# Performance work log

Measured on AMD Instinct MI355X. Metric: run time of the kernel, lower is better.

## Reference

```python
import jax, jax.numpy as jnp
import numpy as np

N = 8192  # num_nodes
E = 8192  # num_edges (== N so self-loops sit on the diagonal)
C = 256   # in_channels
ALPHA = 0.1
BETA = 0.5


def setup_inputs() -> dict:
    key = jax.random.key(0)
    k1, k2, k3 = jax.random.split(key, 3)
    x_0 = jax.random.normal(k1, (N, C), dtype=jnp.float32)
    # binary hypergraph incidence with self-loops on the diagonal
    mask = (jax.random.uniform(k2, (N, E)) < 0.004).astype(jnp.float32)
    idx = jnp.arange(N)
    incidence_1 = mask.at[idx, idx].set(1.0)
    # torch Linear(C, C, bias=False) weight, Kaiming-uniform-ish scale
    W = jax.random.normal(k3, (C, C), dtype=jnp.float32) / jnp.sqrt(C)
    return {"x_0": x_0, "incidence_1": incidence_1, "W": W}


def reference(x_0, incidence_1, W):
    # 1) edge aggregation: m_{0->1} = B^T x  -> [E, C]
    m_0_1 = incidence_1.T @ x_0
    # degree normalization (matches diag/to_dense math without materializing diag)
    node_degree = jnp.sum(incidence_1, axis=1)                      # [N]
    edge_degree = (node_degree @ incidence_1) / jnp.sum(incidence_1, axis=0)  # [E]
    # 2) node aggregation with 1/sqrt(d_z), 1/sqrt(d_x) scaling
    m_1_0 = (incidence_1 @ (m_0_1 / jnp.sqrt(edge_degree)[:, None])) \
            / jnp.sqrt(node_degree)[:, None]                        # [N, C]
    # 3) skip + learned update (x_skip defaults to x_0)
    x_combined = (1.0 - ALPHA) * m_1_0 + ALPHA * x_0
    return (1.0 - BETA) * x_combined + BETA * (x_combined @ W.T)
```

## Files before the change

### kernel.cpp

```cpp
#include <hip/hip_runtime.h>
#include <hip/hip_bf16.h>

#define NN 8192
#define NE 8192
#define CC 256
#define CAP 128

typedef __attribute__((ext_vector_type(8))) short bf16x8;
typedef __attribute__((ext_vector_type(4))) float f32x4;

static __device__ __forceinline__ ushort f2b(float f) {
    unsigned u = __float_as_uint(f);
    return (ushort)((u + 0x7fffu + ((u >> 16) & 1u)) >> 16);
}
static __device__ __forceinline__ float b2f(ushort u) {
    return __uint_as_float((unsigned)u << 16);
}

__global__ __launch_bounds__(256) void k1_scan(const float* __restrict__ B,
                                               const float* __restrict__ x0,
                                               const float* __restrict__ W,
                                               ushort* __restrict__ x0b,
                                               ushort* __restrict__ Wb,
                                               int* __restrict__ csr,
                                               int* __restrict__ row_cnt,
                                               int* __restrict__ col_cnt,
                                               int* __restrict__ csc,
                                               float* __restrict__ edge_wsum) {
    {
        int i = blockIdx.x * 1024 + threadIdx.x * 4;
        float4 v = *(const float4*)(x0 + i);
        ushort4 u; u.x = f2b(v.x); u.y = f2b(v.y); u.z = f2b(v.z); u.w = f2b(v.w);
        *(ushort4*)(x0b + i) = u;
        if (blockIdx.x < 64) {
            float4 w = *(const float4*)(W + i);
            ushort4 uw; uw.x = f2b(w.x); uw.y = f2b(w.y); uw.z = f2b(w.z); uw.w = f2b(w.w);
            *(ushort4*)(Wb + i) = uw;
        }
    }
    const int wave = threadIdx.x >> 6;
    const int lane = threadIdx.x & 63;
    const int row  = blockIdx.x * 4 + wave;
    const float4* rp = (const float4*)(B + (size_t)row * NE);
    int* outp = csr + (size_t)row * CAP;
    const unsigned long long mlt = (1ull << lane) - 1ull;
    int base = 0;
    for (int it = 0; it < NE / 256; ++it) {
        float4 v = rp[it * 64 + lane];
        unsigned long long bx = __ballot(v.x != 0.f);
        unsigned long long by = __ballot(v.y != 0.f);
        unsigned long long bz = __ballot(v.z != 0.f);
        unsigned long long bw = __ballot(v.w != 0.f);
        if (!(bx | by | bz | bw)) continue;
        int tx = __popcll(bx), ty = __popcll(by), tz = __popcll(bz), tw = __popcll(bw);
        int e0 = (it * 64 + lane) * 4;
        int p;
        if (v.x != 0.f) { p = base + __popcll(bx & mlt);                if (p < CAP) outp[p] = e0;     }
        if (v.y != 0.f) { p = base + tx + __popcll(by & mlt);           if (p < CAP) outp[p] = e0 + 1; }
        if (v.z != 0.f) { p = base + tx + ty + __popcll(bz & mlt);      if (p < CAP) outp[p] = e0 + 2; }
        if (v.w != 0.f) { p = base + tx + ty + tz + __popcll(bw & mlt); if (p < CAP) outp[p] = e0 + 3; }
        base += tx + ty + tz + tw;
    }
    const int cnt = base < CAP ? base : CAP;
    if (lane == 0) row_cnt[row] = cnt;
    const float deg = (float)cnt;
    for (int i = lane; i < cnt; i += 64) {
        int e = outp[i];
        int pos = atomicAdd(&col_cnt[e], 1);
        if (pos < CAP) csc[(size_t)e * CAP + pos] = row;
        atomicAdd(&edge_wsum[e], deg);
    }
}

__global__ __launch_bounds__(256) void k4_edge_agg(const ushort* __restrict__ x0b,
                                                   const int* __restrict__ csc,
                                                   const int* __restrict__ col_cnt,
                                                   const float* __restrict__ edge_wsum,
                                                   ushort* __restrict__ m01s) {
    const int wave = threadIdx.x >> 6;
    const int lane = threadIdx.x & 63;
    const int e = blockIdx.x * 4 + wave;
    int cnt = col_cnt[e]; if (cnt > CAP) cnt = CAP;
    const float er = rsqrtf(edge_wsum[e] / (float)cnt);
    const int* cp = csc + (size_t)e * CAP;
    const int idx = cp[lane];
    const ushort* xb = x0b + lane * 4;
    float ax = 0.f, ay = 0.f, az = 0.f, aw = 0.f;
    float bx = 0.f, by = 0.f, bz = 0.f, bw = 0.f;
    const int lim = cnt < 64 ? cnt : 64;
    int i = 0;
    for (; i + 2 <= lim; i += 2) {
        int n0 = __shfl(idx, i), n1 = __shfl(idx, i + 1);
        ushort4 a = *(const ushort4*)(xb + (size_t)n0 * CC);
        ushort4 b = *(const ushort4*)(xb + (size_t)n1 * CC);
        ax += b2f(a.x); ay += b2f(a.y); az += b2f(a.z); aw += b2f(a.w);
        bx += b2f(b.x); by += b2f(b.y); bz += b2f(b.z); bw += b2f(b.w);
    }
    if (i < lim) {
        int n = __shfl(idx, i);
        ushort4 a = *(const ushort4*)(xb + (size_t)n * CC);
        ax += b2f(a.x); ay += b2f(a.y); az += b2f(a.z); aw += b2f(a.w);
    }
    for (int j = 64; j < cnt; ++j) {
        int n = cp[j];
        ushort4 a = *(const ushort4*)(xb + (size_t)n * CC);
        ax += b2f(a.x); ay += b2f(a.y); az += b2f(a.z); aw += b2f(a.w);
    }
    ushort4 r;
    r.x = f2b((ax + bx) * er); r.y = f2b((ay + by) * er);
    r.z = f2b((az + bz) * er); r.w = f2b((aw + bw) * er);
    *(ushort4*)(m01s + (size_t)e * CC + lane * 4) = r;
}

__global__ __launch_bounds__(256) void k5_node_agg(const ushort* __restrict__ x0b,
                                                   const ushort* __restrict__ m01s,
                                                   const int* __restrict__ csr,
                                                   const int* __restrict__ row_cnt,
                                                   ushort* __restrict__ xcb) {
    const int wave = threadIdx.x >> 6;
    const int lane = threadIdx.x & 63;
    const int n = blockIdx.x * 4 + wave;
    const int cnt = row_cnt[n];
    const float nr = rsqrtf((float)cnt);
    const int* ep = csr + (size_t)n * CAP;
    const int idx = ep[lane];
    const ushort* mb = m01s + lane * 4;
    float ax = 0.f, ay = 0.f, az = 0.f, aw = 0.f;
    float bx = 0.f, by = 0.f, bz = 0.f, bw = 0.f;
    const int lim = cnt < 64 ? cnt : 64;
    int i = 0;
    for (; i + 2 <= lim; i += 2) {
        int e0 = __shfl(idx, i), e1 = __shfl(idx, i + 1);
        ushort4 a = *(const ushort4*)(mb + (size_t)e0 * CC);
        ushort4 b = *(const ushort4*)(mb + (size_t)e1 * CC);
        ax += b2f(a.x); ay += b2f(a.y); az += b2f(a.z); aw += b2f(a.w);
        bx += b2f(b.x); by += b2f(b.y); bz += b2f(b.z); bw += b2f(b.w);
    }
    if (i < lim) {
        int e0 = __shfl(idx, i);
        ushort4 a = *(const ushort4*)(mb + (size_t)e0 * CC);
        ax += b2f(a.x); ay += b2f(a.y); az += b2f(a.z); aw += b2f(a.w);
    }
    for (int j = 64; j < cnt; ++j) {
        int e0 = ep[j];
        ushort4 a = *(const ushort4*)(mb + (size_t)e0 * CC);
        ax += b2f(a.x); ay += b2f(a.y); az += b2f(a.z); aw += b2f(a.w);
    }
    ushort4 x = *(const ushort4*)(x0b + (size_t)n * CC + lane * 4);
    const float s = 0.9f * nr;
    ushort4 r;
    r.x = f2b(s * (ax + bx) + 0.1f * b2f(x.x));
    r.y = f2b(s * (ay + by) + 0.1f * b2f(x.y));
    r.z = f2b(s * (az + bz) + 0.1f * b2f(x.z));
    r.w = f2b(s * (aw + bw) + 0.1f * b2f(x.w));
    *(ushort4*)(xcb + (size_t)n * CC + lane * 4) = r;
}

__global__ __launch_bounds__(256) void k6_gemm(const ushort* __restrict__ xcb,
                                               const ushort* __restrict__ Wb,
                                               float* __restrict__ out) {
    const int lane = threadIdx.x & 63;
    const int gw = blockIdx.x * 4 + (threadIdx.x >> 6);
    const int m0 = (gw >> 2) * 16;
    const int n0 = (gw & 3) * 64;
    const int lr = lane & 15, lk = lane >> 4;
    f32x4 acc[4] = {};
    const ushort* ap = xcb + (size_t)(m0 + lr) * CC + lk * 8;
    #pragma unroll
    for (int kb = 0; kb < 8; ++kb) {
        bf16x8 a = *(const bf16x8*)(ap + kb * 32);
        #pragma unroll
        for (int j = 0; j < 4; ++j) {
            bf16x8 b = *(const bf16x8*)(Wb + (size_t)(n0 + j * 16 + lr) * CC + kb * 32 + lk * 8);
            acc[j] = __builtin_amdgcn_mfma_f32_16x16x32_bf16(a, b, acc[j], 0, 0, 0);
        }
    }
    #pragma unroll
    for (int j = 0; j < 4; ++j) {
        #pragma unroll
        for (int r = 0; r < 4; ++r) {
            int row = m0 + lk * 4 + r;
            int col = n0 + j * 16 + lr;
            float sk = b2f(xcb[(size_t)row * CC + col]);
            out[(size_t)row * CC + col] = 0.5f * sk + 0.5f * acc[j][r];
        }
    }
}

extern "C" void kernel_launch(void* const* d_in, const int* in_sizes, int n_in,
                              void* d_out, int out_size, void* d_ws, size_t ws_size,
                              hipStream_t stream) {
    const float* x0 = (const float*)d_in[0];
    const float* B  = (const float*)d_in[1];
    const float* W  = (const float*)d_in[2];
    float* out = (float*)d_out;

    char* ws = (char*)d_ws;
    const size_t need = (21ull << 20) + 4ull * NE * 4;
    if (ws_size < need) return;

    int*    csr       = (int*)(ws);
    int*    csc       = (int*)(ws + (4ull << 20));
    ushort* m01s      = (ushort*)(ws + (8ull << 20));
    ushort* xcb       = (ushort*)(ws + (12ull << 20));
    ushort* x0b       = (ushort*)(ws + (16ull << 20));
    ushort* Wb        = (ushort*)(ws + (20ull << 20));
    int*    row_cnt   = (int*)(ws + (20ull << 20) + (256u << 10));
    int*    col_cnt   = row_cnt + NN;
    float*  edge_wsum = (float*)(col_cnt + NE);

    hipMemsetAsync(col_cnt, 0, 2ull * NE * 4, stream);

    k1_scan<<<NN / 4, 256, 0, stream>>>(B, x0, W, x0b, Wb, csr, row_cnt, col_cnt, csc, edge_wsum);
    k4_edge_agg<<<NE / 4, 256, 0, stream>>>(x0b, csc, col_cnt, edge_wsum, m01s);
    k5_node_agg<<<NN / 4, 256, 0, stream>>>(x0b, m01s, csr, row_cnt, xcb);
    k6_gemm<<<NN * CC / 16 / 64 / 4, 256, 0, stream>>>(xcb, Wb, out);
}
```

Measured before the change: 114.6 us.

## Fuse node aggregation with GEMM and widen gather loads to 16 bytes

The node-aggregation kernel and the W GEMM are merged into one kernel. Each 1024-thread block aggregates 16 node rows into shared memory, then its 16 waves each compute a 16-column MFMA tile, so the bf16 xcb round trip and one launch go away. Both gather kernels now use 8-element bf16 loads, with each half-wave handling a different neighbour, and combine the halves with a cross-lane shuffle. The cost is that every block reloads all of W from global or L2 memory, and the large blocks with a barrier may lower occupancy.

```diff
diff --git a/kernel.cpp b/kernel.cpp
--- a/kernel.cpp
+++ b/kernel.cpp
@@ -7,6 +7,7 @@
 #define CAP 128
 
 typedef __attribute__((ext_vector_type(8))) short bf16x8;
+typedef __attribute__((ext_vector_type(8))) unsigned short u16x8;
 typedef __attribute__((ext_vector_type(4))) float f32x4;
 
 static __device__ __forceinline__ ushort f2b(float f) {
@@ -79,111 +80,136 @@
                                                    ushort* __restrict__ m01s) {
     const int wave = threadIdx.x >> 6;
     const int lane = threadIdx.x & 63;
+    const int half = lane >> 5;
+    const int cl = lane & 31;
     const int e = blockIdx.x * 4 + wave;
     int cnt = col_cnt[e]; if (cnt > CAP) cnt = CAP;
     const float er = rsqrtf(edge_wsum[e] / (float)cnt);
     const int* cp = csc + (size_t)e * CAP;
     const int idx = cp[lane];
-    const ushort* xb = x0b + lane * 4;
-    float ax = 0.f, ay = 0.f, az = 0.f, aw = 0.f;
-    float bx = 0.f, by = 0.f, bz = 0.f, bw = 0.f;
+    const ushort* xb = x0b + cl * 8;
+    float a0[8] = {}, a1[8] = {};
     const int lim = cnt < 64 ? cnt : 64;
     int i = 0;
-    for (; i + 2 <= lim; i += 2) {
-        int n0 = __shfl(idx, i), n1 = __shfl(idx, i + 1);
-        ushort4 a = *(const ushort4*)(xb + (size_t)n0 * CC);
-        ushort4 b = *(const ushort4*)(xb + (size_t)n1 * CC);
-        ax += b2f(a.x); ay += b2f(a.y); az += b2f(a.z); aw += b2f(a.w);
-        bx += b2f(b.x); by += b2f(b.y); bz += b2f(b.z); bw += b2f(b.w);
+    for (; i + 4 <= lim; i += 4) {
+        int na = __shfl(idx, i + half);
+        int nb = __shfl(idx, i + 2 + half);
+        u16x8 a = *(const u16x8*)(xb + (size_t)na * CC);
+        u16x8 b = *(const u16x8*)(xb + (size_t)nb * CC);
+        #pragma unroll
+        for (int c = 0; c < 8; ++c) { a0[c] += b2f(a[c]); a1[c] += b2f(b[c]); }
+    }
+    if (i + 2 <= lim) {
+        int na = __shfl(idx, i + half);
+        u16x8 a = *(const u16x8*)(xb + (size_t)na * CC);
+        #pragma unroll
+        for (int c = 0; c < 8; ++c) a0[c] += b2f(a[c]);
+        i += 2;
     }
     if (i < lim) {
-        int n = __shfl(idx, i);
-        ushort4 a = *(const ushort4*)(xb + (size_t)n * CC);
-        ax += b2f(a.x); ay += b2f(a.y); az += b2f(a.z); aw += b2f(a.w);
-    }
-    for (int j = 64; j < cnt; ++j) {
-        int n = cp[j];
-        ushort4 a = *(const ushort4*)(xb + (size_t)n * CC);
-        ax += b2f(a.x); ay += b2f(a.y); az += b2f(a.z); aw += b2f(a.w);
-    }
-    ushort4 r;
-    r.x = f2b((ax + bx) * er); r.y = f2b((ay + by) * er);
-    r.z = f2b((az + bz) * er); r.w = f2b((aw + bw) * er);
-    *(ushort4*)(m01s + (size_t)e * CC + lane * 4) = r;
-}
-
-__global__ __launch_bounds__(256) void k5_node_agg(const ushort* __restrict__ x0b,
-                                                   const ushort* __restrict__ m01s,
-                                                   const int* __restrict__ csr,
-                                                   const int* __restrict__ row_cnt,
-                                                   ushort* __restrict__ xcb) {
-    const int wave = threadIdx.x >> 6;
+        int na = __shfl(idx, i);
+        if (half == 0) {
+            u16x8 a = *(const u16x8*)(xb + (size_t)na * CC);
+            #pragma unroll
+            for (int c = 0; c < 8; ++c) a0[c] += b2f(a[c]);
+        }
+    }
+    if (cnt > 64 && half == 0) {
+        for (int j = 64; j < cnt; ++j) {
+            int n2 = cp[j];
+            u16x8 a = *(const u16x8*)(xb + (size_t)n2 * CC);
+            #pragma unroll
+            for (int c = 0; c < 8; ++c) a0[c] += b2f(a[c]);
+        }
+    }
+    u16x8 r8;
+    #pragma unroll
+    for (int c = 0; c < 8; ++c) {
+        float t = a0[c] + a1[c];
+        t += __shfl_xor(t, 32);
+        r8[c] = f2b(t * er);
+    }
+    if (half == 0) *(u16x8*)(m01s + (size_t)e * CC + cl * 8) = r8;
+}
+
+__global__ __launch_bounds__(1024, 8) void k5_fused(const ushort* __restrict__ x0b,
+                                                    const ushort* __restrict__ m01s,
+                                                    const int* __restrict__ csr,
+                                                    const int* __restrict__ row_cnt,
+                                                    const ushort* __restrict__ Wb,
+                                                    float* __restrict__ out) {
+    __shared__ __align__(16) ushort xs[16][264];
+    const int w = threadIdx.x >> 6;
     const int lane = threadIdx.x & 63;
-    const int n = blockIdx.x * 4 + wave;
+    const int half = lane >> 5;
+    const int cl = lane & 31;
+    const int n = blockIdx.x * 16 + w;
     const int cnt = row_cnt[n];
     const float nr = rsqrtf((float)cnt);
     const int* ep = csr + (size_t)n * CAP;
     const int idx = ep[lane];
-    const ushort* mb = m01s + lane * 4;
-    float ax = 0.f, ay = 0.f, az = 0.f, aw = 0.f;
-    float bx = 0.f, by = 0.f, bz = 0.f, bw = 0.f;
+    const ushort* mb = m01s + cl * 8;
+    float a0[8] = {}, a1[8] = {};
     const int lim = cnt < 64 ? cnt : 64;
     int i = 0;
-    for (; i + 2 <= lim; i += 2) {
-        int e0 = __shfl(idx, i), e1 = __shfl(idx, i + 1);
-        ushort4 a = *(const ushort4*)(mb + (size_t)e0 * CC);
-        ushort4 b = *(const ushort4*)(mb + (size_t)e1 * CC);
-        ax += b2f(a.x); ay += b2f(a.y); az += b2f(a.z); aw += b2f(a.w);
-        bx += b2f(b.x); by += b2f(b.y); bz += b2f(b.z); bw += b2f(b.w);
+    for (; i + 4 <= lim; i += 4) {
+        int ea = __shfl(idx, i + half);
+        int eb = __shfl(idx, i + 2 + half);
+        u16x8 a = *(const u16x8*)(mb + (size_t)ea * CC);
+        u16x8 b = *(const u16x8*)(mb + (size_t)eb * CC);
+        #pragma unroll
+        for (int c = 0; c < 8; ++c) { a0[c] += b2f(a[c]); a1[c] += b2f(b[c]); }
+    }
+    if (i + 2 <= lim) {
+        int ea = __shfl(idx, i + half);
+        u16x8 a = *(const u16x8*)(mb + (size_t)ea * CC);
+        #pragma unroll
+        for (int c = 0; c < 8; ++c) a0[c] += b2f(a[c]);
+        i += 2;
     }
     if (i < lim) {
-        int e0 = __shfl(idx, i);
-        ushort4 a = *(const ushort4*)(mb + (size_t)e0 * CC);
-        ax += b2f(a.x); ay += b2f(a.y); az += b2f(a.z); aw += b2f(a.w);
-    }
-    for (int j = 64; j < cnt; ++j) {
-        int e0 = ep[j];
-        ushort4 a = *(const ushort4*)(mb + (size_t)e0 * CC);
-        ax += b2f(a.x); ay += b2f(a.y); az += b2f(a.z); aw += b2f(a.w);
-    }
-    ushort4 x = *(const ushort4*)(x0b + (size_t)n * CC + lane * 4);
+        int ea = __shfl(idx, i);
+        if (half == 0) {
+            u16x8 a = *(const u16x8*)(mb + (size_t)ea * CC);
+            #pragma unroll
+            for (int c = 0; c < 8; ++c) a0[c] += b2f(a[c]);
+        }
+    }
+    if (cnt > 64 && half == 0) {
+        for (int j = 64; j < cnt; ++j) {
+            int e2 = ep[j];
+            u16x8 a = *(const u16x8*)(mb + (size_t)e2 * CC);
+            #pragma unroll
+            for (int c = 0; c < 8; ++c) a0[c] += b2f(a[c]);
+        }
+    }
+    u16x8 x = *(const u16x8*)(x0b + (size_t)n * CC + cl * 8);
     const float s = 0.9f * nr;
-    ushort4 r;
-    r.x = f2b(s * (ax + bx) + 0.1f * b2f(x.x));
-    r.y = f2b(s * (ay + by) + 0.1f * b2f(x.y));
-    r.z = f2b(s * (az + bz) + 0.1f * b2f(x.z));
-    r.w = f2b(s * (aw + bw) + 0.1f * b2f(x.w));
-    *(ushort4*)(xcb + (size_t)n * CC + lane * 4) = r;
-}
-
-__global__ __launch_bounds__(256) void k6_gemm(const ushort* __restrict__ xcb,
-                                               const ushort* __restrict__ Wb,
-                                               float* __restrict__ out) {
-    const int lane = threadIdx.x & 63;
-    const int gw = blockIdx.x * 4 + (threadIdx.x >> 6);
-    const int m0 = (gw >> 2) * 16;
-    const int n0 = (gw & 3) * 64;
+    u16x8 r8;
+    #pragma unroll
+    for (int c = 0; c < 8; ++c) {
+        float t = a0[c] + a1[c];
+        t += __shfl_xor(t, 32);
+        r8[c] = f2b(s * t + 0.1f * b2f(x[c]));
+    }
+    if (half == 0) *(u16x8*)(&xs[w][cl * 8]) = r8;
+    __syncthreads();
     const int lr = lane & 15, lk = lane >> 4;
-    f32x4 acc[4] = {};
-    const ushort* ap = xcb + (size_t)(m0 + lr) * CC + lk * 8;
+    const int n0 = w * 16;
+    f32x4 acc = {0.f, 0.f, 0.f, 0.f};
     #pragma unroll
     for (int kb = 0; kb < 8; ++kb) {
-        bf16x8 a = *(const bf16x8*)(ap + kb * 32);
-        #pragma unroll
-        for (int j = 0; j < 4; ++j) {
-            bf16x8 b = *(const bf16x8*)(Wb + (size_t)(n0 + j * 16 + lr) * CC + kb * 32 + lk * 8);
-            acc[j] = __builtin_amdgcn_mfma_f32_16x16x32_bf16(a, b, acc[j], 0, 0, 0);
-        }
-    }
-    #pragma unroll
-    for (int j = 0; j < 4; ++j) {
-        #pragma unroll
-        for (int r = 0; r < 4; ++r) {
-            int row = m0 + lk * 4 + r;
-            int col = n0 + j * 16 + lr;
-            float sk = b2f(xcb[(size_t)row * CC + col]);
-            out[(size_t)row * CC + col] = 0.5f * sk + 0.5f * acc[j][r];
-        }
+        bf16x8 a = *(const bf16x8*)(&xs[lr][kb * 32 + lk * 8]);
+        bf16x8 b = *(const bf16x8*)(Wb + (size_t)(n0 + lr) * CC + kb * 32 + lk * 8);
+        acc = __builtin_amdgcn_mfma_f32_16x16x32_bf16(a, b, acc, 0, 0, 0);
+    }
+    const size_t rb = (size_t)blockIdx.x * 16;
+    #pragma unroll
+    for (int r = 0; r < 4; ++r) {
+        int row = lk * 4 + r;
+        int col = n0 + lr;
+        float sk = b2f(xs[row][col]);
+        out[(rb + row) * CC + col] = 0.5f * sk + 0.5f * acc[r];
     }
 }
 
@@ -196,16 +222,15 @@
     float* out = (float*)d_out;
 
     char* ws = (char*)d_ws;
-    const size_t need = (21ull << 20) + 4ull * NE * 4;
+    const size_t need = (17ull << 20) + 4ull * NE * 4;
     if (ws_size < need) return;
 
     int*    csr       = (int*)(ws);
     int*    csc       = (int*)(ws + (4ull << 20));
     ushort* m01s      = (ushort*)(ws + (8ull << 20));
-    ushort* xcb       = (ushort*)(ws + (12ull << 20));
-    ushort* x0b       = (ushort*)(ws + (16ull << 20));
-    ushort* Wb        = (ushort*)(ws + (20ull << 20));
-    int*    row_cnt   = (int*)(ws + (20ull << 20) + (256u << 10));
+    ushort* x0b       = (ushort*)(ws + (12ull << 20));
+    ushort* Wb        = (ushort*)(ws + (16ull << 20));
+    int*    row_cnt   = (int*)(ws + (16ull << 20) + (256u << 10));
     int*    col_cnt   = row_cnt + NN;
     float*  edge_wsum = (float*)(col_cnt + NE);
 
@@ -213,6 +238,5 @@
 
     k1_scan<<<NN / 4, 256, 0, stream>>>(B, x0, W, x0b, Wb, csr, row_cnt, col_cnt, csc, edge_wsum);
     k4_edge_agg<<<NE / 4, 256, 0, stream>>>(x0b, csc, col_cnt, edge_wsum, m01s);
-    k5_node_agg<<<NN / 4, 256, 0, stream>>>(x0b, m01s, csr, row_cnt, xcb);
-    k6_gemm<<<NN * CC / 16 / 64 / 4, 256, 0, stream>>>(xcb, Wb, out);
-}
+    k5_fused<<<NN / 16, 1024, 0, stream>>>(x0b, m01s, csr, row_cnt, Wb, out);
+}
```

Measured after the change: 104.7 us. -8.6%, faster.
